# Performance work log

Hardware: AMD Instinct MI355X
Metric: run time of the kernel (lower is better)

The kernel has to match this reference:

```python
import jax, jax.numpy as jnp
import numpy as np

N_NODES = 100000
N_EDGES = 1600000
D = 64
N_LAYERS = 5  # hops=4 -> hops+1 GraphConv layers


def setup_inputs() -> dict:
    key = jax.random.key(0)
    k1, k2, k3, k4, k5, k6 = jax.random.split(key, 6)
    x = jax.random.normal(k1, (N_NODES, D), dtype=jnp.float32)
    edge_index = jax.random.randint(k2, (2, N_EDGES), 0, N_NODES, dtype=jnp.int64)
    edge_weight = jax.random.uniform(k3, (N_EDGES,), dtype=jnp.float32)
    # Per-layer params (all dims are 64 so we can stack): PyG GraphConv has
    # lin_rel (with bias) applied to the aggregated messages and lin_root
    # (no bias) applied to the node's own features.
    scale = 1.0 / np.sqrt(D)
    W_rel = jax.random.normal(k4, (N_LAYERS, D, D), dtype=jnp.float32) * scale
    b_rel = jnp.zeros((N_LAYERS, D), dtype=jnp.float32)
    W_root = jax.random.normal(k5, (N_LAYERS, D, D), dtype=jnp.float32) * scale
    return {"x": x, "edge_index": edge_index, "edge_weight": edge_weight,
            "W_rel": W_rel, "b_rel": b_rel, "W_root": W_root}


def _graph_conv(x, src, dst, edge_weight, W_rel_i, b_rel_i, W_root_i):
    # message: x_j * w_e ; aggregate: scatter-add onto destination nodes
    msg = x[src] * edge_weight[:, None]               # [E, D] gather
    agg = jax.ops.segment_sum(msg, dst, num_segments=N_NODES)  # [N, D] scatter
    return agg @ W_rel_i + b_rel_i + x @ W_root_i


def reference(x, edge_index, edge_weight, W_rel, b_rel, W_root):
    src, dst = edge_index[0], edge_index[1]
    h = x
    for i in range(N_LAYERS - 1):
        h = _graph_conv(h, src, dst, edge_weight, W_rel[i], b_rel[i], W_root[i])
        h = jax.nn.relu(h)
    h = _graph_conv(h, src, dst, edge_weight, W_rel[-1], b_rel[-1], W_root[-1])
    return h
```

## Files before the change

### kernel.cpp

```cpp
#include <hip/hip_runtime.h>

#define N_NODES 100000
#define N_EDGES 1600000
#define D 64
#define N_LAYERS 5
#define FB 1000
#define BN 100
#define NX 8
#define BCAP_X 320
#define BCAP 2048
#define BIN_BLOCKS 512
#define BIN_THREADS 512
#define BIN_CHUNK 3125

typedef unsigned short u16;
typedef unsigned long long u64;
typedef __attribute__((ext_vector_type(8))) short bf16x8;
typedef __attribute__((ext_vector_type(4))) float f32x4;

__device__ __forceinline__ float bf2f(u16 u) {
    union { unsigned int i; float f; } v;
    v.i = ((unsigned int)u) << 16;
    return v.f;
}
__device__ __forceinline__ u16 f2bf(float f) {
    union { float f; unsigned int i; } v;
    v.f = f;
    unsigned int r = v.i + 0x7FFFu + ((v.i >> 16) & 1u);
    return (u16)(r >> 16);
}
__device__ __forceinline__ float bf2f_lo(unsigned int pk) {
    union { unsigned int i; float f; } v;
    v.i = pk << 16;
    return v.f;
}
__device__ __forceinline__ float bf2f_hi(unsigned int pk) {
    union { unsigned int i; float f; } v;
    v.i = pk & 0xFFFF0000u;
    return v.f;
}


__global__ __launch_bounds__(1024) void initcur_kernel(int* __restrict__ fcur)
{
    int i = blockIdx.x * 1024 + threadIdx.x;
    if (i < NX * FB) fcur[i] = i * BCAP_X;
}

__global__ __launch_bounds__(BIN_THREADS) void bin_kernel(
    const int* __restrict__ src, const int* __restrict__ dst,
    const float* __restrict__ ew, int* __restrict__ fcur,
    u64* __restrict__ stag)
{
    __shared__ int hc[FB];
    const int xbase = (blockIdx.x & (NX - 1)) * FB;
    for (int b = threadIdx.x; b < FB; b += BIN_THREADS) hc[b] = 0;
    __syncthreads();
    const int e0 = blockIdx.x * BIN_CHUNK;
    for (int e = e0 + threadIdx.x; e < e0 + BIN_CHUNK; e += BIN_THREADS) {
        int d = dst[e];
        atomicAdd(&hc[d / BN], 1);
    }
    __syncthreads();
    for (int b = threadIdx.x; b < FB; b += BIN_THREADS) {
        int c = hc[b];
        if (c) hc[b] = atomicAdd(&fcur[xbase + b], c);
    }
    __syncthreads();
    for (int e = e0 + threadIdx.x; e < e0 + BIN_CHUNK; e += BIN_THREADS) {
        int d = dst[e];
        int b = d / BN;
        int pos = atomicAdd(&hc[b], 1);
        int s   = __builtin_nontemporal_load(&src[e]);
        float w = __builtin_nontemporal_load(&ew[e]);
        unsigned int pk = (unsigned int)((d - b * BN) << 17) | (unsigned int)s;
        u64 rec = ((u64)(unsigned int)__float_as_int(w) << 32) | pk;
        stag[pos] = rec;
    }
}

__global__ __launch_bounds__(1024) void fscan_kernel(
    const int* __restrict__ fcur, int* __restrict__ fbase,
    int* __restrict__ rowptr)
{
    __shared__ int s[1024];
    int t = threadIdx.x;
    int v = 0;
    if (t < FB) {
        #pragma unroll
        for (int x = 0; x < NX; ++x) {
            int cell = x * FB + t;
            v += fcur[cell] - cell * BCAP_X;
        }
    }
    s[t] = v;
    __syncthreads();
    for (int off = 1; off < 1024; off <<= 1) {
        int u = (t >= off) ? s[t - off] : 0;
        __syncthreads();
        s[t] += u;
        __syncthreads();
    }
    if (t < FB) fbase[t] = s[t] - v;
    if (t == FB - 1) {
        fbase[FB] = s[t];
        rowptr[N_NODES] = s[t];
    }
}

__global__ __launch_bounds__(256) void sort_kernel(
    const u64* __restrict__ stag, const int* __restrict__ fcur,
    const int* __restrict__ fbase, int* __restrict__ rowptr,
    int2* __restrict__ edges)
{
    __shared__ u64 ls[BCAP];
    __shared__ int cnt[BN];
    __shared__ int cur[BN];
    __shared__ int sc[128];
    const int b = blockIdx.x;
    const int base = fbase[b];
    const int t = threadIdx.x;
    for (int i = t; i < BN; i += 256) cnt[i] = 0;
    __syncthreads();
    int ofs = 0;
    #pragma unroll
    for (int x = 0; x < NX; ++x) {
        int cell = x * FB + b;
        int sz = fcur[cell] - cell * BCAP_X;
        const u64* sp = stag + (size_t)cell * BCAP_X;
        for (int i = t; i < sz; i += 256) {
            u64 r = __builtin_nontemporal_load(&sp[i]);
            ls[ofs + i] = r;
            atomicAdd(&cnt[((unsigned int)r) >> 17], 1);
        }
        ofs += sz;
    }
    const int size = ofs;
    __syncthreads();
    if (t < 128) sc[t] = (t < BN) ? cnt[t] : 0;
    __syncthreads();
    for (int off = 1; off < 128; off <<= 1) {
        int u = 0;
        if (t < 128 && t >= off) u = sc[t - off];
        __syncthreads();
        if (t < 128) sc[t] += u;
        __syncthreads();
    }
    if (t < BN) {
        int excl = sc[t] - cnt[t];
        rowptr[b * BN + t] = base + excl;
        cur[t] = excl;
    }
    __syncthreads();
    for (int i = t; i < size; i += 256) {
        u64 r = ls[i];
        unsigned int lo = (unsigned int)r;
        int dloc = lo >> 17;
        int rank = atomicAdd(&cur[dloc], 1);
        edges[base + rank] = make_int2((int)(lo & 0x1FFFFu),
                                       (int)(unsigned int)(r >> 32));
    }
}

__global__ __launch_bounds__(256) void f2bf_kernel(
    const float* __restrict__ in, u16* __restrict__ out)
{
    int i = blockIdx.x * 256 + threadIdx.x;
    if (i >= (N_NODES * D) / 4) return;
    float4 v = ((const float4*)in)[i];
    ushort4 o;
    o.x = f2bf(v.x); o.y = f2bf(v.y); o.z = f2bf(v.z); o.w = f2bf(v.w);
    ((ushort4*)out)[i] = o;
}

__global__ __launch_bounds__(256) void wprep_kernel(
    const float* __restrict__ Wrel, const float* __restrict__ Wroot,
    u16* __restrict__ W2T)
{
    int i = blockIdx.x * 256 + threadIdx.x;
    if (i >= N_LAYERS * 64 * 128) return;
    int l = i / (64 * 128);
    int rem = i % (64 * 128);
    int n = rem >> 7;
    int k = rem & 127;
    float v = (k < 64) ? Wrel[l * 4096 + k * 64 + n]
                       : Wroot[l * 4096 + (k - 64) * 64 + n];
    W2T[i] = f2bf(v);
}

__global__ __launch_bounds__(256) void agg_kernel(
    const u16* __restrict__ h, const int* __restrict__ rowptr,
    const int2* __restrict__ edges, u16* __restrict__ agg)
{
    int wid  = (blockIdx.x * 256 + threadIdx.x) >> 6;
    int lane = threadIdx.x & 63;
    int sl   = lane & 31;
    int node = wid * 2 + (lane >> 5);
    if (node >= N_NODES) return;
    int b = rowptr[node];
    int e = rowptr[node + 1];
    float acc0 = 0.f, acc1 = 0.f;
    for (int base = b; base < e; base += 32) {
        int cnt = min(32, e - base);
        int idx = 0;
        float wv = 0.f;
        if (sl < cnt) {
            int2 p = edges[base + sl];
            idx = p.x;
            wv = __int_as_float(p.y);
        }
        int j = 0;
        for (; j + 8 <= cnt; j += 8) {
            int s0 = __shfl(idx, j + 0, 32), s1 = __shfl(idx, j + 1, 32);
            int s2 = __shfl(idx, j + 2, 32), s3 = __shfl(idx, j + 3, 32);
            int s4 = __shfl(idx, j + 4, 32), s5 = __shfl(idx, j + 5, 32);
            int s6 = __shfl(idx, j + 6, 32), s7 = __shfl(idx, j + 7, 32);
            float w0 = __shfl(wv, j + 0, 32), w1 = __shfl(wv, j + 1, 32);
            float w2 = __shfl(wv, j + 2, 32), w3 = __shfl(wv, j + 3, 32);
            float w4 = __shfl(wv, j + 4, 32), w5 = __shfl(wv, j + 5, 32);
            float w6 = __shfl(wv, j + 6, 32), w7 = __shfl(wv, j + 7, 32);
            unsigned int p0 = *(const unsigned int*)(h + ((size_t)s0 << 6) + sl * 2);
            unsigned int p1 = *(const unsigned int*)(h + ((size_t)s1 << 6) + sl * 2);
            unsigned int p2 = *(const unsigned int*)(h + ((size_t)s2 << 6) + sl * 2);
            unsigned int p3 = *(const unsigned int*)(h + ((size_t)s3 << 6) + sl * 2);
            unsigned int p4 = *(const unsigned int*)(h + ((size_t)s4 << 6) + sl * 2);
            unsigned int p5 = *(const unsigned int*)(h + ((size_t)s5 << 6) + sl * 2);
            unsigned int p6 = *(const unsigned int*)(h + ((size_t)s6 << 6) + sl * 2);
            unsigned int p7 = *(const unsigned int*)(h + ((size_t)s7 << 6) + sl * 2);
            acc0 += bf2f_lo(p0) * w0 + bf2f_lo(p1) * w1
                  + bf2f_lo(p2) * w2 + bf2f_lo(p3) * w3
                  + bf2f_lo(p4) * w4 + bf2f_lo(p5) * w5
                  + bf2f_lo(p6) * w6 + bf2f_lo(p7) * w7;
            acc1 += bf2f_hi(p0) * w0 + bf2f_hi(p1) * w1
                  + bf2f_hi(p2) * w2 + bf2f_hi(p3) * w3
                  + bf2f_hi(p4) * w4 + bf2f_hi(p5) * w5
                  + bf2f_hi(p6) * w6 + bf2f_hi(p7) * w7;
        }
        for (; j < cnt; ++j) {
            int s = __shfl(idx, j, 32);
            float w = __shfl(wv, j, 32);
            unsigned int pk = *(const unsigned int*)(h + ((size_t)s << 6) + sl * 2);
            acc0 += bf2f_lo(pk) * w;
            acc1 += bf2f_hi(pk) * w;
        }
    }
    unsigned int o = ((unsigned int)f2bf(acc1) << 16) | f2bf(acc0);
    *(unsigned int*)(agg + ((size_t)node << 6) + sl * 2) = o;
}

__global__ __launch_bounds__(256) void update_mfma_kernel(
    const u16* __restrict__ hin, const u16* __restrict__ agg,
    const u16* __restrict__ W2T, const float* __restrict__ brel,
    u16* __restrict__ hout_bf, float* __restrict__ hout_f32, int relu)
{
    const int wave = threadIdx.x >> 6;
    const int lane = threadIdx.x & 63;
    const int nb16 = blockIdx.x * 64 + wave * 16;
    const int m = lane & 15;
    const int q = lane >> 4;

    int anode = nb16 + m;
    size_t rowa = (size_t)((anode < N_NODES) ? anode : 0) << 6;

    bf16x8 a[4];
    a[0] = *(const bf16x8*)(agg + rowa + q * 8);
    a[1] = *(const bf16x8*)(agg + rowa + 32 + q * 8);
    a[2] = *(const bf16x8*)(hin + rowa + q * 8);
    a[3] = *(const bf16x8*)(hin + rowa + 32 + q * 8);

    bf16x8 bfr[4][4];
    #pragma unroll
    for (int nt = 0; nt < 4; ++nt)
        #pragma unroll
        for (int kk = 0; kk < 4; ++kk)
            bfr[nt][kk] = *(const bf16x8*)(W2T + (size_t)(nt * 16 + m) * 128
                                           + kk * 32 + q * 8);

    f32x4 acc[4];
    #pragma unroll
    for (int nt = 0; nt < 4; ++nt) {
        float bv = brel[nt * 16 + m];
        acc[nt] = (f32x4){bv, bv, bv, bv};
    }

    #pragma unroll
    for (int kk = 0; kk < 4; ++kk)
        #pragma unroll
        for (int nt = 0; nt < 4; ++nt)
            acc[nt] = __builtin_amdgcn_mfma_f32_16x16x32_bf16(
                a[kk], bfr[nt][kk], acc[nt], 0, 0, 0);

    #pragma unroll
    for (int nt = 0; nt < 4; ++nt)
        #pragma unroll
        for (int r = 0; r < 4; ++r) {
            int n2 = nb16 + q * 4 + r;
            if (n2 < N_NODES) {
                float v = acc[nt][r];
                if (relu) v = fmaxf(v, 0.f);
                int dim = nt * 16 + m;
                if (hout_f32) hout_f32[(size_t)n2 * 64 + dim] = v;
                else          hout_bf [(size_t)n2 * 64 + dim] = f2bf(v);
            }
        }
}

extern "C" void kernel_launch(void* const* d_in, const int* in_sizes, int n_in,
                              void* d_out, int out_size, void* d_ws, size_t ws_size,
                              hipStream_t stream)
{
    const float* x     = (const float*)d_in[0];
    const int*   ei    = (const int*)d_in[1];
    const float* ew    = (const float*)d_in[2];
    const float* Wrel  = (const float*)d_in[3];
    const float* brel  = (const float*)d_in[4];
    const float* Wroot = (const float*)d_in[5];
    float* out = (float*)d_out;

    const int* src = ei;
    const int* dst = ei + N_EDGES;

    const size_t featb_bytes = (size_t)N_NODES * D * 2;
    char* ws = (char*)d_ws;
    size_t off = 0;
    u16*  hb     = (u16*)(ws + off);  off += featb_bytes;
    u16*  aggb   = (u16*)(ws + off);  off += featb_bytes;
    u16*  W2T    = (u16*)(ws + off);  off += (size_t)N_LAYERS * 64 * 128 * 2;
    int*  rowptr = (int*)(ws + off);  off += 400016;
    int*  fcur   = (int*)(ws + off);  off += NX * FB * 4;
    int*  fbase  = (int*)(ws + off);  off += (FB + 1) * 4 + 60;
    int2* edges  = (int2*)(ws + off); off += (size_t)N_EDGES * 8;

    u64* stag = (u64*)ws;

    const int cblocks = (N_NODES * D / 4 + 255) / 256;
    const int wblocks = (N_LAYERS * 64 * 128 + 255) / 256;
    const int ablocks = ((N_NODES + 1) / 2 + 3) / 4;
    const int ublocks = (N_NODES + 63) / 64;

    initcur_kernel<<<8, 1024, 0, stream>>>(fcur);
    bin_kernel<<<BIN_BLOCKS, BIN_THREADS, 0, stream>>>(src, dst, ew, fcur, stag);
    fscan_kernel<<<1, 1024, 0, stream>>>(fcur, fbase, rowptr);
    sort_kernel<<<FB, 256, 0, stream>>>(stag, fcur, fbase, rowptr, edges);
    f2bf_kernel<<<cblocks, 256, 0, stream>>>(x, hb);
    wprep_kernel<<<wblocks, 256, 0, stream>>>(Wrel, Wroot, W2T);

    for (int layer = 0; layer < N_LAYERS; ++layer) {
        agg_kernel<<<ablocks, 256, 0, stream>>>(hb, rowptr, edges, aggb);
        int last = (layer == N_LAYERS - 1);
        update_mfma_kernel<<<ublocks, 256, 0, stream>>>(
            hb, aggb, W2T + (size_t)layer * 64 * 128,
            brel + (size_t)layer * D,
            last ? nullptr : hb, last ? out : nullptr,
            last ? 0 : 1);
    }
}
```

Baseline: 412.8 us.

## Fuse neighbor aggregation and MFMA update into a single per-layer kernel

Merges the gather-aggregate kernel and the MFMA update kernel into one layer kernel. Each wave aggregates its 16 nodes into a swizzled LDS tile, which then serves directly as the MFMA A-operand. This removes the global write and read of the aggregated feature buffer and one launch per layer. Node features now ping-pong between two buffers, since the fused kernel reads neighbor rows while other blocks write outputs. The trade-off is far fewer waves in flight, with each wave aggregating 16 nodes in sequence, which may weaken latency hiding for the random gathers.

```diff
diff --git a/kernel.cpp b/kernel.cpp
--- a/kernel.cpp
+++ b/kernel.cpp
@@ -188,83 +188,89 @@
     W2T[i] = f2bf(v);
 }
 
-__global__ __launch_bounds__(256) void agg_kernel(
-    const u16* __restrict__ h, const int* __restrict__ rowptr,
-    const int2* __restrict__ edges, u16* __restrict__ agg)
-{
-    int wid  = (blockIdx.x * 256 + threadIdx.x) >> 6;
-    int lane = threadIdx.x & 63;
-    int sl   = lane & 31;
-    int node = wid * 2 + (lane >> 5);
-    if (node >= N_NODES) return;
-    int b = rowptr[node];
-    int e = rowptr[node + 1];
-    float acc0 = 0.f, acc1 = 0.f;
-    for (int base = b; base < e; base += 32) {
-        int cnt = min(32, e - base);
-        int idx = 0;
-        float wv = 0.f;
-        if (sl < cnt) {
-            int2 p = edges[base + sl];
-            idx = p.x;
-            wv = __int_as_float(p.y);
-        }
-        int j = 0;
-        for (; j + 8 <= cnt; j += 8) {
-            int s0 = __shfl(idx, j + 0, 32), s1 = __shfl(idx, j + 1, 32);
-            int s2 = __shfl(idx, j + 2, 32), s3 = __shfl(idx, j + 3, 32);
-            int s4 = __shfl(idx, j + 4, 32), s5 = __shfl(idx, j + 5, 32);
-            int s6 = __shfl(idx, j + 6, 32), s7 = __shfl(idx, j + 7, 32);
-            float w0 = __shfl(wv, j + 0, 32), w1 = __shfl(wv, j + 1, 32);
-            float w2 = __shfl(wv, j + 2, 32), w3 = __shfl(wv, j + 3, 32);
-            float w4 = __shfl(wv, j + 4, 32), w5 = __shfl(wv, j + 5, 32);
-            float w6 = __shfl(wv, j + 6, 32), w7 = __shfl(wv, j + 7, 32);
-            unsigned int p0 = *(const unsigned int*)(h + ((size_t)s0 << 6) + sl * 2);
-            unsigned int p1 = *(const unsigned int*)(h + ((size_t)s1 << 6) + sl * 2);
-            unsigned int p2 = *(const unsigned int*)(h + ((size_t)s2 << 6) + sl * 2);
-            unsigned int p3 = *(const unsigned int*)(h + ((size_t)s3 << 6) + sl * 2);
-            unsigned int p4 = *(const unsigned int*)(h + ((size_t)s4 << 6) + sl * 2);
-            unsigned int p5 = *(const unsigned int*)(h + ((size_t)s5 << 6) + sl * 2);
-            unsigned int p6 = *(const unsigned int*)(h + ((size_t)s6 << 6) + sl * 2);
-            unsigned int p7 = *(const unsigned int*)(h + ((size_t)s7 << 6) + sl * 2);
-            acc0 += bf2f_lo(p0) * w0 + bf2f_lo(p1) * w1
-                  + bf2f_lo(p2) * w2 + bf2f_lo(p3) * w3
-                  + bf2f_lo(p4) * w4 + bf2f_lo(p5) * w5
-                  + bf2f_lo(p6) * w6 + bf2f_lo(p7) * w7;
-            acc1 += bf2f_hi(p0) * w0 + bf2f_hi(p1) * w1
-                  + bf2f_hi(p2) * w2 + bf2f_hi(p3) * w3
-                  + bf2f_hi(p4) * w4 + bf2f_hi(p5) * w5
-                  + bf2f_hi(p6) * w6 + bf2f_hi(p7) * w7;
-        }
-        for (; j < cnt; ++j) {
-            int s = __shfl(idx, j, 32);
-            float w = __shfl(wv, j, 32);
-            unsigned int pk = *(const unsigned int*)(h + ((size_t)s << 6) + sl * 2);
-            acc0 += bf2f_lo(pk) * w;
-            acc1 += bf2f_hi(pk) * w;
-        }
-    }
-    unsigned int o = ((unsigned int)f2bf(acc1) << 16) | f2bf(acc0);
-    *(unsigned int*)(agg + ((size_t)node << 6) + sl * 2) = o;
-}
-
-__global__ __launch_bounds__(256) void update_mfma_kernel(
-    const u16* __restrict__ hin, const u16* __restrict__ agg,
-    const u16* __restrict__ W2T, const float* __restrict__ brel,
+__global__ __launch_bounds__(256) void layer_kernel(
+    const u16* __restrict__ hin, const int* __restrict__ rowptr,
+    const int2* __restrict__ edges, const u16* __restrict__ W2T,
+    const float* __restrict__ brel,
     u16* __restrict__ hout_bf, float* __restrict__ hout_f32, int relu)
 {
+    __shared__ u16 aggs[4][16][64];
     const int wave = threadIdx.x >> 6;
     const int lane = threadIdx.x & 63;
     const int nb16 = blockIdx.x * 64 + wave * 16;
+    const int sl   = lane & 31;
+    const int half = lane >> 5;
+    u16* wtile = &aggs[wave][0][0];
+
+    for (int t = 0; t < 8; ++t) {
+        int nl = 2 * t + half;
+        int node = nb16 + nl;
+        float acc0 = 0.f, acc1 = 0.f;
+        if (node < N_NODES) {
+            int b = rowptr[node];
+            int e = rowptr[node + 1];
+            for (int base = b; base < e; base += 32) {
+                int cnt = min(32, e - base);
+                int idx = 0;
+                float wv = 0.f;
+                if (sl < cnt) {
+                    int2 p = edges[base + sl];
+                    idx = p.x;
+                    wv = __int_as_float(p.y);
+                }
+                int j = 0;
+                for (; j + 8 <= cnt; j += 8) {
+                    int s0 = __shfl(idx, j + 0, 32), s1 = __shfl(idx, j + 1, 32);
+                    int s2 = __shfl(idx, j + 2, 32), s3 = __shfl(idx, j + 3, 32);
+                    int s4 = __shfl(idx, j + 4, 32), s5 = __shfl(idx, j + 5, 32);
+                    int s6 = __shfl(idx, j + 6, 32), s7 = __shfl(idx, j + 7, 32);
+                    float w0 = __shfl(wv, j + 0, 32), w1 = __shfl(wv, j + 1, 32);
+                    float w2 = __shfl(wv, j + 2, 32), w3 = __shfl(wv, j + 3, 32);
+                    float w4 = __shfl(wv, j + 4, 32), w5 = __shfl(wv, j + 5, 32);
+                    float w6 = __shfl(wv, j + 6, 32), w7 = __shfl(wv, j + 7, 32);
+                    unsigned int p0 = *(const unsigned int*)(hin + ((size_t)s0 << 6) + sl * 2);
+                    unsigned int p1 = *(const unsigned int*)(hin + ((size_t)s1 << 6) + sl * 2);
+                    unsigned int p2 = *(const unsigned int*)(hin + ((size_t)s2 << 6) + sl * 2);
+                    unsigned int p3 = *(const unsigned int*)(hin + ((size_t)s3 << 6) + sl * 2);
+                    unsigned int p4 = *(const unsigned int*)(hin + ((size_t)s4 << 6) + sl * 2);
+                    unsigned int p5 = *(const unsigned int*)(hin + ((size_t)s5 << 6) + sl * 2);
+                    unsigned int p6 = *(const unsigned int*)(hin + ((size_t)s6 << 6) + sl * 2);
+                    unsigned int p7 = *(const unsigned int*)(hin + ((size_t)s7 << 6) + sl * 2);
+                    acc0 += bf2f_lo(p0) * w0 + bf2f_lo(p1) * w1
+                          + bf2f_lo(p2) * w2 + bf2f_lo(p3) * w3
+                          + bf2f_lo(p4) * w4 + bf2f_lo(p5) * w5
+                          + bf2f_lo(p6) * w6 + bf2f_lo(p7) * w7;
+                    acc1 += bf2f_hi(p0) * w0 + bf2f_hi(p1) * w1
+                          + bf2f_hi(p2) * w2 + bf2f_hi(p3) * w3
+                          + bf2f_hi(p4) * w4 + bf2f_hi(p5) * w5
+                          + bf2f_hi(p6) * w6 + bf2f_hi(p7) * w7;
+                }
+                for (; j < cnt; ++j) {
+                    int s = __shfl(idx, j, 32);
+                    float w = __shfl(wv, j, 32);
+                    unsigned int pk = *(const unsigned int*)(hin + ((size_t)s << 6) + sl * 2);
+                    acc0 += bf2f_lo(pk) * w;
+                    acc1 += bf2f_hi(pk) * w;
+                }
+            }
+        }
+        int u16idx = (nl << 6) | ((sl * 2) ^ ((nl & 7) << 3));
+        unsigned int o = ((unsigned int)f2bf(acc1) << 16) | f2bf(acc0);
+        *(unsigned int*)(wtile + u16idx) = o;
+    }
+
     const int m = lane & 15;
     const int q = lane >> 4;
 
+    bf16x8 a[4];
+    {
+        int r0 = (m << 6) | ((q * 8) ^ ((m & 7) << 3));
+        int r1 = (m << 6) | ((32 + q * 8) ^ ((m & 7) << 3));
+        a[0] = *(const bf16x8*)(wtile + r0);
+        a[1] = *(const bf16x8*)(wtile + r1);
+    }
     int anode = nb16 + m;
     size_t rowa = (size_t)((anode < N_NODES) ? anode : 0) << 6;
-
-    bf16x8 a[4];
-    a[0] = *(const bf16x8*)(agg + rowa + q * 8);
-    a[1] = *(const bf16x8*)(agg + rowa + 32 + q * 8);
     a[2] = *(const bf16x8*)(hin + rowa + q * 8);
     a[3] = *(const bf16x8*)(hin + rowa + 32 + q * 8);
 
@@ -324,7 +330,7 @@
     char* ws = (char*)d_ws;
     size_t off = 0;
     u16*  hb     = (u16*)(ws + off);  off += featb_bytes;
-    u16*  aggb   = (u16*)(ws + off);  off += featb_bytes;
+    u16*  hb2    = (u16*)(ws + off);  off += featb_bytes;
     u16*  W2T    = (u16*)(ws + off);  off += (size_t)N_LAYERS * 64 * 128 * 2;
     int*  rowptr = (int*)(ws + off);  off += 400016;
     int*  fcur   = (int*)(ws + off);  off += NX * FB * 4;
@@ -333,10 +339,11 @@
 
     u64* stag = (u64*)ws;
 
+    u16* hbuf[2] = {hb, hb2};
+
     const int cblocks = (N_NODES * D / 4 + 255) / 256;
     const int wblocks = (N_LAYERS * 64 * 128 + 255) / 256;
-    const int ablocks = ((N_NODES + 1) / 2 + 3) / 4;
-    const int ublocks = (N_NODES + 63) / 64;
+    const int lblocks = (N_NODES + 63) / 64;
 
     initcur_kernel<<<8, 1024, 0, stream>>>(fcur);
     bin_kernel<<<BIN_BLOCKS, BIN_THREADS, 0, stream>>>(src, dst, ew, fcur, stag);
@@ -346,12 +353,13 @@
     wprep_kernel<<<wblocks, 256, 0, stream>>>(Wrel, Wroot, W2T);
 
     for (int layer = 0; layer < N_LAYERS; ++layer) {
-        agg_kernel<<<ablocks, 256, 0, stream>>>(hb, rowptr, edges, aggb);
         int last = (layer == N_LAYERS - 1);
-        update_mfma_kernel<<<ublocks, 256, 0, stream>>>(
-            hb, aggb, W2T + (size_t)layer * 64 * 128,
+        layer_kernel<<<lblocks, 256, 0, stream>>>(
+            hbuf[layer & 1], rowptr, edges,
+            W2T + (size_t)layer * 64 * 128,
             brel + (size_t)layer * D,
-            last ? nullptr : hb, last ? out : nullptr,
+            last ? nullptr : hbuf[(layer + 1) & 1],
+            last ? out : nullptr,
             last ? 0 : 1);
     }
 }
```

Result: slower. 472.5 us (+14.5%).
